# Kernel optimization log

Hardware: AMD Instinct MI355X
Metric: run time of the kernel (lower is better)

The kernel has to match this reference:

```python
import jax, jax.numpy as jnp
import numpy as np

DIM = 768
NUM_HEADS = 12
HEAD_DIM = DIM // NUM_HEADS
SCALE = HEAD_DIM ** -0.5


def setup_inputs() -> dict:
    key = jax.random.key(0)
    k1, k2, k3 = jax.random.split(key, 3)
    B, N = 4, 2048
    x = jax.random.normal(k1, (B, N, DIM), dtype=jnp.float32)
    qkv_w = jax.random.normal(k2, (3 * DIM, DIM), dtype=jnp.float32) * (DIM ** -0.5)
    proj_w = jax.random.normal(k3, (DIM, DIM), dtype=jnp.float32) * (DIM ** -0.5)
    proj_b = jnp.zeros((DIM,), dtype=jnp.float32)
    return {"x": x, "qkv_w": qkv_w, "proj_w": proj_w, "proj_b": proj_b}


def reference(x, qkv_w, proj_w, proj_b):
    B, N, C = x.shape
    # qkv projection (no bias; qkv_bias=False)
    qkv = jnp.einsum('bnc,dc->bnd', x, qkv_w)               # [B,N,3C]
    qkv = qkv.reshape(B, N, 3, NUM_HEADS, HEAD_DIM)
    qkv = jnp.transpose(qkv, (2, 0, 3, 1, 4))               # [3,B,H,N,Dh]
    q, k, v = qkv[0] * SCALE, qkv[1], qkv[2]
    attn = jnp.einsum('bhqd,bhkd->bhqk', q, k)              # [B,H,N,N]
    attn = jax.nn.softmax(attn, axis=-1)
    out = jnp.einsum('bhqk,bhkd->bhqd', attn, v)            # [B,H,N,Dh]
    out = jnp.transpose(out, (0, 2, 1, 3)).reshape(B, N, C)
    out = jnp.einsum('bnc,dc->bnd', out, proj_w) + proj_b
    return out
```

## Files before the change

### kernel.cpp

```cpp
#include <hip/hip_runtime.h>
#include <cstdint>
#include <cstddef>

typedef __attribute__((ext_vector_type(8))) short short8v;
typedef __attribute__((ext_vector_type(4))) float f32x4;
typedef __attribute__((ext_vector_type(16))) float f32x16;
typedef __attribute__((ext_vector_type(4))) unsigned int u32x4;
typedef unsigned short us;

#define GLL16(gsrc, ldst)                                                           \
  __builtin_amdgcn_global_load_lds((__attribute__((address_space(1))) void*)(gsrc), \
                                   (__attribute__((address_space(3))) void*)(ldst), \
                                   16, 0, 0)

#define MFMA32(a, b, c) __builtin_amdgcn_mfma_f32_32x32x16_bf16((a), (b), (c), 0, 0, 0)

static __device__ __forceinline__ us f2bf(float f) {
  unsigned int u = __float_as_uint(f);
  u += 0x7FFFu + ((u >> 16) & 1u);
  return (us)(u >> 16);
}

static __device__ __forceinline__ unsigned int cvtpk_bf16(float lo, float hi) {
  unsigned int r;
  asm("v_cvt_pk_bf16_f32 %0, %1, %2" : "=v"(r) : "v"(lo), "v"(hi));
  return r;
}

template <int B>
static __device__ __forceinline__ short8v pack_swap(const f32x16& p) {
  unsigned int X = cvtpk_bf16(p[B + 0], p[B + 1]);
  unsigned int Y = cvtpk_bf16(p[B + 2], p[B + 3]);
  unsigned int Z = cvtpk_bf16(p[B + 4], p[B + 5]);
  unsigned int W = cvtpk_bf16(p[B + 6], p[B + 7]);
  asm("v_permlane32_swap_b32 %0, %1" : "+v"(X), "+v"(Z));
  asm("v_permlane32_swap_b32 %0, %1" : "+v"(Y), "+v"(W));
  u32x4 f;
  f.x = X; f.y = Y; f.z = Z; f.w = W;
  return __builtin_bit_cast(short8v, f);
}

static __device__ __forceinline__ u32x4 cvt8(const float4 a, const float4 b) {
  u32x4 u;
  u.x = cvtpk_bf16(a.x, a.y);
  u.y = cvtpk_bf16(a.z, a.w);
  u.z = cvtpk_bf16(b.x, b.y);
  u.w = cvtpk_bf16(b.z, b.w);
  return u;
}

__global__ __launch_bounds__(256, 3)
void gemm_qkv(const float* __restrict__ A32, const float* __restrict__ B32,
              int M, int N, int K,
              us* __restrict__ qout, us* __restrict__ kout, us* __restrict__ vtout)
{
  __shared__ us SH[2][2][128 * 32];

  const int tid  = threadIdx.x;
  const int lane = tid & 63;
  const int w    = tid >> 6;
  const int g    = lane >> 4;
  const int c    = lane & 15;
  const int wr   = w >> 1;
  const int wc   = w & 1;
  const int ntn  = N >> 7;

  const int nwg  = (M >> 7) * ntn;
  const int cpx  = nwg >> 3;
  const int bid  = (blockIdx.x & 7) * cpx + (blockIdx.x >> 3);
  const int tm   = bid / ntn;
  const int tn   = bid - tm * ntn;
  const int row_a0 = tm * 128;
  const int col_b0 = tn * 128;

  f32x4 acc[4][4];
#pragma unroll
  for (int i = 0; i < 4; ++i)
#pragma unroll
    for (int j = 0; j < 4; ++j) acc[i][j] = (f32x4){0.f, 0.f, 0.f, 0.f};

  float4 ra[2][2], rb[2][2];

#define STAGE_LOAD(ks)                                                        \
  do {                                                                        \
    _Pragma("unroll")                                                         \
    for (int p = 0; p < 2; ++p) {                                             \
      int G = p * 256 + tid, row = G >> 2, kslot = G & 3;                     \
      const float* s = A32 + (size_t)(row_a0 + row) * K + (ks) * 32 + kslot * 8; \
      ra[p][0] = *(const float4*)s;  ra[p][1] = *(const float4*)(s + 4);      \
    }                                                                         \
    _Pragma("unroll")                                                         \
    for (int p = 0; p < 2; ++p) {                                             \
      int G = p * 256 + tid, row = G >> 2, kslot = G & 3;                     \
      const float* s = B32 + (size_t)(col_b0 + row) * K + (ks) * 32 + kslot * 8; \
      rb[p][0] = *(const float4*)s;  rb[p][1] = *(const float4*)(s + 4);      \
    }                                                                         \
  } while (0)

#define STAGE_WRITE(buf)                                                      \
  do {                                                                        \
    _Pragma("unroll")                                                         \
    for (int p = 0; p < 2; ++p) {                                             \
      int G = p * 256 + tid, row = G >> 2, kslot = G & 3;                     \
      *(u32x4*)&SH[buf][0][(kslot * 128 + row) * 8] = cvt8(ra[p][0], ra[p][1]); \
      *(u32x4*)&SH[buf][1][(kslot * 128 + row) * 8] = cvt8(rb[p][0], rb[p][1]); \
    }                                                                         \
  } while (0)

  const int nt = K >> 5;
  STAGE_LOAD(0);
  STAGE_WRITE(0);
  __syncthreads();

  for (int t = 0; t < nt; ++t) {
    const int cur = t & 1;
    if (t + 1 < nt) STAGE_LOAD(t + 1);

    short8v af[4], bfr[4];
#pragma unroll
    for (int mi = 0; mi < 4; ++mi)
      af[mi] = *(const short8v*)&SH[cur][0][(g * 128 + wr * 64 + mi * 16 + c) * 8];
#pragma unroll
    for (int nj = 0; nj < 4; ++nj)
      bfr[nj] = *(const short8v*)&SH[cur][1][(g * 128 + wc * 64 + nj * 16 + c) * 8];
    __builtin_amdgcn_s_setprio(1);
#pragma unroll
    for (int mi = 0; mi < 4; ++mi)
#pragma unroll
      for (int nj = 0; nj < 4; ++nj)
        acc[mi][nj] = __builtin_amdgcn_mfma_f32_16x16x32_bf16(af[mi], bfr[nj], acc[mi][nj], 0, 0, 0);
    __builtin_amdgcn_s_setprio(0);

    if (t + 1 < nt) STAGE_WRITE(cur ^ 1);
    __syncthreads();
  }
#undef STAGE_LOAD
#undef STAGE_WRITE

  const int rbase = row_a0 + wr * 64;
  const int cbase = col_b0 + wc * 64;
  if (cbase < 1536) {
#pragma unroll
    for (int mi = 0; mi < 4; ++mi)
#pragma unroll
      for (int nj = 0; nj < 4; ++nj)
#pragma unroll
        for (int r = 0; r < 4; ++r) {
          float v   = acc[mi][nj][r];
          int mrow  = rbase + mi * 16 + g * 4 + r;
          int d     = cbase + nj * 16 + c;
          int hh    = d < 768 ? (d >> 6) : ((d - 768) >> 6);
          int dh    = d & 63;
          int b     = mrow >> 11, n = mrow & 2047;
          size_t bh = (size_t)(b * 12 + hh);
          if (d < 768) qout[(bh * 2048 + n) * 64 + dh] = f2bf(v * 0.18033688f);
          else         kout[(bh * 2048 + n) * 64 + dh] = f2bf(v);
        }
  } else {
    us* Lw = &SH[0][0][0] + w * (64 * 40);
    const int b   = rbase >> 11;
    const int nl0 = rbase & 2047;
    const int h2  = (cbase - 1536) >> 6;
    const size_t vrow0 = ((size_t)(b * 12 + h2)) * 64;
#pragma unroll
    for (int pass = 0; pass < 2; ++pass) {
#pragma unroll
      for (int mi2 = 0; mi2 < 2; ++mi2) {
        int mi = pass * 2 + mi2;
#pragma unroll
        for (int nj = 0; nj < 4; ++nj)
#pragma unroll
          for (int r = 0; r < 4; ++r)
            Lw[(nj * 16 + c) * 40 + mi2 * 16 + g * 4 + r] = f2bf(acc[mi][nj][r]);
      }
#pragma unroll
      for (int p = 0; p < 4; ++p) {
        int G   = p * 64 + lane;
        int dl  = G >> 2;
        int seg = G & 3;
        short8v vv = *(const short8v*)&Lw[dl * 40 + seg * 8];
        *(short8v*)(vtout + (vrow0 + dl) * 2048 + nl0 + pass * 32 + seg * 8) = vv;
      }
    }
  }
}

__global__ __launch_bounds__(256, 3)
void gemm_proj(const us* __restrict__ A, const float* __restrict__ B32,
               int M, int N, int K,
               const float* __restrict__ bias, float* __restrict__ fout)
{
  __shared__ us SH[2][2][128 * 32];

  const int tid  = threadIdx.x;
  const int lane = tid & 63;
  const int w    = tid >> 6;
  const int g    = lane >> 4;
  const int c    = lane & 15;
  const int wr   = w >> 1;
  const int wc   = w & 1;
  const int ntn  = N >> 7;

  const int nwg  = (M >> 7) * ntn;
  const int cpx  = nwg >> 3;
  const int bid  = (blockIdx.x & 7) * cpx + (blockIdx.x >> 3);
  const int tm   = bid / ntn;
  const int tn   = bid - tm * ntn;
  const int row_a0 = tm * 128;
  const int col_b0 = tn * 128;

  f32x4 acc[4][4];
#pragma unroll
  for (int i = 0; i < 4; ++i)
#pragma unroll
    for (int j = 0; j < 4; ++j) acc[i][j] = (f32x4){0.f, 0.f, 0.f, 0.f};

  float4 rb[2][2];

#define STAGE_A(buf, ks)                                                      \
  do {                                                                        \
    _Pragma("unroll")                                                         \
    for (int p = 0; p < 2; ++p) {                                             \
      int G = p * 256 + tid;                                                  \
      int kslot = G >> 7, row = G & 127;                                      \
      GLL16(A + (size_t)(row_a0 + row) * K + (ks) * 32 + kslot * 8,           \
            &SH[buf][0][G * 8]);                                              \
    }                                                                         \
  } while (0)

#define STAGE_B_LOAD(ks)                                                      \
  do {                                                                        \
    _Pragma("unroll")                                                         \
    for (int p = 0; p < 2; ++p) {                                             \
      int G = p * 256 + tid, row = G >> 2, kslot = G & 3;                     \
      const float* s = B32 + (size_t)(col_b0 + row) * K + (ks) * 32 + kslot * 8; \
      rb[p][0] = *(const float4*)s;  rb[p][1] = *(const float4*)(s + 4);      \
    }                                                                         \
  } while (0)

#define STAGE_B_WRITE(buf)                                                    \
  do {                                                                        \
    _Pragma("unroll")                                                         \
    for (int p = 0; p < 2; ++p) {                                             \
      int G = p * 256 + tid, row = G >> 2, kslot = G & 3;                     \
      *(u32x4*)&SH[buf][1][(kslot * 128 + row) * 8] = cvt8(rb[p][0], rb[p][1]); \
    }                                                                         \
  } while (0)

  const int nt = K >> 5;
  STAGE_A(0, 0);
  STAGE_B_LOAD(0);
  STAGE_B_WRITE(0);
  __syncthreads();

  for (int t = 0; t < nt; ++t) {
    const int cur = t & 1;
    if (t + 1 < nt) { STAGE_A(cur ^ 1, t + 1); STAGE_B_LOAD(t + 1); }

    short8v af[4], bfr[4];
#pragma unroll
    for (int mi = 0; mi < 4; ++mi)
      af[mi] = *(const short8v*)&SH[cur][0][(g * 128 + wr * 64 + mi * 16 + c) * 8];
#pragma unroll
    for (int nj = 0; nj < 4; ++nj)
      bfr[nj] = *(const short8v*)&SH[cur][1][(g * 128 + wc * 64 + nj * 16 + c) * 8];
    __builtin_amdgcn_s_setprio(1);
#pragma unroll
    for (int mi = 0; mi < 4; ++mi)
#pragma unroll
      for (int nj = 0; nj < 4; ++nj)
        acc[mi][nj] = __builtin_amdgcn_mfma_f32_16x16x32_bf16(af[mi], bfr[nj], acc[mi][nj], 0, 0, 0);
    __builtin_amdgcn_s_setprio(0);

    if (t + 1 < nt) STAGE_B_WRITE(cur ^ 1);
    __syncthreads();
  }
#undef STAGE_A
#undef STAGE_B_LOAD
#undef STAGE_B_WRITE

  const int rbase = row_a0 + wr * 64;
  const int cbase = col_b0 + wc * 64;
#pragma unroll
  for (int mi = 0; mi < 4; ++mi)
#pragma unroll
    for (int nj = 0; nj < 4; ++nj) {
      int d = cbase + nj * 16 + c;
      float bv = bias[d];
#pragma unroll
      for (int r = 0; r < 4; ++r) {
        int mrow = rbase + mi * 16 + g * 4 + r;
        fout[(size_t)mrow * N + d] = acc[mi][nj][r] + bv;
      }
    }
}

__global__ __launch_bounds__(256, 3)
void attn_fwd(const us* __restrict__ Qg, const us* __restrict__ Kg,
              const us* __restrict__ Vg, us* __restrict__ Og)
{
  __shared__ us Ks[2][8 * 64 * 8];
  __shared__ us Vs[2][8 * 64 * 8];

  const int tid  = threadIdx.x;
  const int lane = tid & 63;
  const int w    = tid >> 6;
  const int q31  = lane & 31;
  const int hi   = lane >> 5;

  const int lin = blockIdx.x;
  const int xcd = lin & 7;
  const int idx = lin >> 3;
  const int bh  = xcd * 6 + (idx >> 4);
  const int qt  = idx & 15;
  const int b   = bh / 12;
  const int h   = bh - b * 12;

  const size_t qrow0 = (size_t)bh * 2048 + qt * 128 + w * 32;

  short8v qf[4];
#pragma unroll
  for (int dc = 0; dc < 4; ++dc)
    qf[dc] = *(const short8v*)(Qg + (qrow0 + q31) * 64 + dc * 16 + hi * 8);

  short8v ones;
#pragma unroll
  for (int j = 0; j < 8; ++j) ones[j] = (short)0x3F80;

  f32x16 o0, o1, ls, z16;
#pragma unroll
  for (int r = 0; r < 16; ++r) { o0[r] = 0.f; o1[r] = 0.f; ls[r] = 0.f; z16[r] = 0.f; }

  const size_t kbase = (size_t)bh * 2048 * 64;
  const size_t vbase = (size_t)bh * 64 * 2048;

#define STAGE_KV(buf, kv0)                                             \
  do {                                                                 \
    _Pragma("unroll")                                                  \
    for (int p = 0; p < 2; ++p) {                                      \
      int G = p * 256 + tid;                                           \
      int kslot = G >> 6, row = G & 63;                                \
      GLL16(Kg + kbase + (size_t)((kv0) + row) * 64 + kslot * 8,       \
            &Ks[buf][(p * 256 + w * 64) * 8]);                         \
    }                                                                  \
    _Pragma("unroll")                                                  \
    for (int p = 0; p < 2; ++p) {                                      \
      int G = p * 256 + tid;                                           \
      int kvslot = G >> 6, dh = G & 63;                                \
      GLL16(Vg + vbase + (size_t)dh * 2048 + (kv0) + kvslot * 8,       \
            &Vs[buf][(p * 256 + w * 64) * 8]);                         \
    }                                                                  \
  } while (0)

  STAGE_KV(0, 0);
  __syncthreads();

  for (int t = 0; t < 32; ++t) {
    const int cur = t & 1;
    if (t < 31) STAGE_KV(cur ^ 1, (t + 1) * 64);

    f32x16 s0, s1;
    __builtin_amdgcn_s_setprio(1);
    {
      const us* kb = &Ks[cur][(hi * 64 + q31) * 8];
      short8v kf0 = *(const short8v*)kb;
      short8v kf1 = *(const short8v*)(kb + 32 * 8);
      s0 = MFMA32(kf0, qf[0], z16);
      s1 = MFMA32(kf1, qf[0], z16);
    }
#pragma unroll
    for (int dc = 1; dc < 4; ++dc) {
      const us* kb = &Ks[cur][((dc * 2 + hi) * 64 + q31) * 8];
      short8v kf0 = *(const short8v*)kb;
      short8v kf1 = *(const short8v*)(kb + 32 * 8);
      s0 = MFMA32(kf0, qf[dc], s0);
      s1 = MFMA32(kf1, qf[dc], s1);
    }
    __builtin_amdgcn_s_setprio(0);

#pragma unroll
    for (int r = 0; r < 16; ++r) {
      s0[r] = __builtin_amdgcn_exp2f(s0[r]);
      s1[r] = __builtin_amdgcn_exp2f(s1[r]);
    }

    short8v pa[4];
    pa[0] = pack_swap<0>(s0);
    pa[1] = pack_swap<8>(s0);
    pa[2] = pack_swap<0>(s1);
    pa[3] = pack_swap<8>(s1);

    __builtin_amdgcn_s_setprio(1);
#pragma unroll
    for (int kc = 0; kc < 4; ++kc) {
      const us* vb = &Vs[cur][((kc * 2 + hi) * 64 + q31) * 8];
      short8v vf0 = *(const short8v*)vb;
      short8v vf1 = *(const short8v*)(vb + 32 * 8);
      o0 = MFMA32(pa[kc], vf0, o0);
      o1 = MFMA32(pa[kc], vf1, o1);
      ls = MFMA32(pa[kc], ones, ls);
    }
    __builtin_amdgcn_s_setprio(0);

    __syncthreads();
  }
#undef STAGE_KV

  const int n0w = qt * 128 + w * 32;
#pragma unroll
  for (int r = 0; r < 16; ++r) {
    float iv = 1.0f / ls[r];
    int n = n0w + (r & 3) + 8 * (r >> 2) + 4 * hi;
    size_t rowbase = ((size_t)b * 2048 + n) * 768 + h * 64 + q31;
    Og[rowbase]      = f2bf(o0[r] * iv);
    Og[rowbase + 32] = f2bf(o1[r] * iv);
  }
}

extern "C" void kernel_launch(void* const* d_in, const int* in_sizes, int n_in,
                              void* d_out, int out_size, void* d_ws, size_t ws_size,
                              hipStream_t stream)
{
  const float* x      = (const float*)d_in[0];
  const float* qkv_w  = (const float*)d_in[1];
  const float* proj_w = (const float*)d_in[2];
  const float* proj_b = (const float*)d_in[3];

  char* ws = (char*)d_ws;
  const size_t SZ_AO   = (size_t)8192 * 768 * 2;
  const size_t SZ_HEAD = (size_t)48 * 2048 * 64;

  us* attn_o = (us*)(ws);
  us* q_bf   = (us*)(ws + SZ_AO);
  us* k_bf   = q_bf + SZ_HEAD;
  us* vt_bf  = k_bf + SZ_HEAD;

  gemm_qkv<<<64 * 18, 256, 0, stream>>>(x, qkv_w, 8192, 2304, 768,
                                        q_bf, k_bf, vt_bf);

  attn_fwd<<<768, 256, 0, stream>>>(q_bf, k_bf, vt_bf, attn_o);

  gemm_proj<<<64 * 6, 256, 0, stream>>>(attn_o, proj_w, 8192, 768, 768,
                                        proj_b, (float*)d_out);
}
```

Baseline: 155.5 us.

## Pre-convert weights to bf16 once and stream them into LDS directly

Adds a small kernel that converts the qkv and projection weights from fp32 to bf16 in the workspace at the start of each call. Both GEMMs then load their weight tiles with global_load_lds straight into shared memory, with no register staging or per-tile conversion. This halves weight read traffic in the GEMM loops and removes conversion ALU work and register pressure. The qkv GEMM's launch bounds are also raised to 4 waves per SIMD. The cost is one extra kernel launch plus a full conversion pass over both weight matrices on every call.

```diff
diff --git a/kernel.cpp b/kernel.cpp
--- a/kernel.cpp
+++ b/kernel.cpp
@@ -49,8 +49,21 @@
   return u;
 }
 
-__global__ __launch_bounds__(256, 3)
-void gemm_qkv(const float* __restrict__ A32, const float* __restrict__ B32,
+__global__ void cvt_w(const float4* __restrict__ i0, ushort4* __restrict__ o0, int n0,
+                      const float4* __restrict__ i1, ushort4* __restrict__ o1, int n1)
+{
+  int i = blockIdx.x * 256 + threadIdx.x;
+  const float4* src;
+  ushort4* dst;
+  if (i < n0)           { src = i0;     dst = o0; }
+  else if (i < n0 + n1) { i -= n0;      src = i1; dst = o1; }
+  else return;
+  float4 v = src[i];
+  dst[i] = make_ushort4(f2bf(v.x), f2bf(v.y), f2bf(v.z), f2bf(v.w));
+}
+
+__global__ __launch_bounds__(256, 4)
+void gemm_qkv(const float* __restrict__ A32, const us* __restrict__ Bw,
               int M, int N, int K,
               us* __restrict__ qout, us* __restrict__ kout, us* __restrict__ vtout)
 {
@@ -79,9 +92,9 @@
 #pragma unroll
     for (int j = 0; j < 4; ++j) acc[i][j] = (f32x4){0.f, 0.f, 0.f, 0.f};
 
-  float4 ra[2][2], rb[2][2];
-
-#define STAGE_LOAD(ks)                                                        \
+  float4 ra[2][2];
+
+#define STAGE_A_LOAD(ks)                                                      \
   do {                                                                        \
     _Pragma("unroll")                                                         \
     for (int p = 0; p < 2; ++p) {                                             \
@@ -89,32 +102,37 @@
       const float* s = A32 + (size_t)(row_a0 + row) * K + (ks) * 32 + kslot * 8; \
       ra[p][0] = *(const float4*)s;  ra[p][1] = *(const float4*)(s + 4);      \
     }                                                                         \
-    _Pragma("unroll")                                                         \
-    for (int p = 0; p < 2; ++p) {                                             \
-      int G = p * 256 + tid, row = G >> 2, kslot = G & 3;                     \
-      const float* s = B32 + (size_t)(col_b0 + row) * K + (ks) * 32 + kslot * 8; \
-      rb[p][0] = *(const float4*)s;  rb[p][1] = *(const float4*)(s + 4);      \
-    }                                                                         \
   } while (0)
 
-#define STAGE_WRITE(buf)                                                      \
+#define STAGE_A_WRITE(buf)                                                    \
   do {                                                                        \
     _Pragma("unroll")                                                         \
     for (int p = 0; p < 2; ++p) {                                             \
       int G = p * 256 + tid, row = G >> 2, kslot = G & 3;                     \
       *(u32x4*)&SH[buf][0][(kslot * 128 + row) * 8] = cvt8(ra[p][0], ra[p][1]); \
-      *(u32x4*)&SH[buf][1][(kslot * 128 + row) * 8] = cvt8(rb[p][0], rb[p][1]); \
     }                                                                         \
   } while (0)
 
+#define STAGE_B(buf, ks)                                                      \
+  do {                                                                        \
+    _Pragma("unroll")                                                         \
+    for (int p = 0; p < 2; ++p) {                                             \
+      int G = p * 256 + tid;                                                  \
+      int kslot = G >> 7, row = G & 127;                                      \
+      GLL16(Bw + (size_t)(col_b0 + row) * K + (ks) * 32 + kslot * 8,          \
+            &SH[buf][1][G * 8]);                                              \
+    }                                                                         \
+  } while (0)
+
   const int nt = K >> 5;
-  STAGE_LOAD(0);
-  STAGE_WRITE(0);
+  STAGE_A_LOAD(0);
+  STAGE_B(0, 0);
+  STAGE_A_WRITE(0);
   __syncthreads();
 
   for (int t = 0; t < nt; ++t) {
     const int cur = t & 1;
-    if (t + 1 < nt) STAGE_LOAD(t + 1);
+    if (t + 1 < nt) { STAGE_B(cur ^ 1, t + 1); STAGE_A_LOAD(t + 1); }
 
     short8v af[4], bfr[4];
 #pragma unroll
@@ -131,11 +149,12 @@
         acc[mi][nj] = __builtin_amdgcn_mfma_f32_16x16x32_bf16(af[mi], bfr[nj], acc[mi][nj], 0, 0, 0);
     __builtin_amdgcn_s_setprio(0);
 
-    if (t + 1 < nt) STAGE_WRITE(cur ^ 1);
+    if (t + 1 < nt) STAGE_A_WRITE(cur ^ 1);
     __syncthreads();
   }
-#undef STAGE_LOAD
-#undef STAGE_WRITE
+#undef STAGE_A_LOAD
+#undef STAGE_A_WRITE
+#undef STAGE_B
 
   const int rbase = row_a0 + wr * 64;
   const int cbase = col_b0 + wc * 64;
@@ -186,7 +205,7 @@
 }
 
 __global__ __launch_bounds__(256, 3)
-void gemm_proj(const us* __restrict__ A, const float* __restrict__ B32,
+void gemm_proj(const us* __restrict__ A, const us* __restrict__ Bw,
                int M, int N, int K,
                const float* __restrict__ bias, float* __restrict__ fout)
 {
@@ -215,9 +234,7 @@
 #pragma unroll
     for (int j = 0; j < 4; ++j) acc[i][j] = (f32x4){0.f, 0.f, 0.f, 0.f};
 
-  float4 rb[2][2];
-
-#define STAGE_A(buf, ks)                                                      \
+#define STAGE_AB(buf, ks)                                                     \
   do {                                                                        \
     _Pragma("unroll")                                                         \
     for (int p = 0; p < 2; ++p) {                                             \
@@ -226,36 +243,22 @@
       GLL16(A + (size_t)(row_a0 + row) * K + (ks) * 32 + kslot * 8,           \
             &SH[buf][0][G * 8]);                                              \
     }                                                                         \
-  } while (0)
-
-#define STAGE_B_LOAD(ks)                                                      \
-  do {                                                                        \
     _Pragma("unroll")                                                         \
     for (int p = 0; p < 2; ++p) {                                             \
-      int G = p * 256 + tid, row = G >> 2, kslot = G & 3;                     \
-      const float* s = B32 + (size_t)(col_b0 + row) * K + (ks) * 32 + kslot * 8; \
-      rb[p][0] = *(const float4*)s;  rb[p][1] = *(const float4*)(s + 4);      \
+      int G = p * 256 + tid;                                                  \
+      int kslot = G >> 7, row = G & 127;                                      \
+      GLL16(Bw + (size_t)(col_b0 + row) * K + (ks) * 32 + kslot * 8,          \
+            &SH[buf][1][G * 8]);                                              \
     }                                                                         \
   } while (0)
 
-#define STAGE_B_WRITE(buf)                                                    \
-  do {                                                                        \
-    _Pragma("unroll")                                                         \
-    for (int p = 0; p < 2; ++p) {                                             \
-      int G = p * 256 + tid, row = G >> 2, kslot = G & 3;                     \
-      *(u32x4*)&SH[buf][1][(kslot * 128 + row) * 8] = cvt8(rb[p][0], rb[p][1]); \
-    }                                                                         \
-  } while (0)
-
   const int nt = K >> 5;
-  STAGE_A(0, 0);
-  STAGE_B_LOAD(0);
-  STAGE_B_WRITE(0);
+  STAGE_AB(0, 0);
   __syncthreads();
 
   for (int t = 0; t < nt; ++t) {
     const int cur = t & 1;
-    if (t + 1 < nt) { STAGE_A(cur ^ 1, t + 1); STAGE_B_LOAD(t + 1); }
+    if (t + 1 < nt) STAGE_AB(cur ^ 1, t + 1);
 
     short8v af[4], bfr[4];
 #pragma unroll
@@ -272,12 +275,9 @@
         acc[mi][nj] = __builtin_amdgcn_mfma_f32_16x16x32_bf16(af[mi], bfr[nj], acc[mi][nj], 0, 0, 0);
     __builtin_amdgcn_s_setprio(0);
 
-    if (t + 1 < nt) STAGE_B_WRITE(cur ^ 1);
     __syncthreads();
   }
-#undef STAGE_A
-#undef STAGE_B_LOAD
-#undef STAGE_B_WRITE
+#undef STAGE_AB
 
   const int rbase = row_a0 + wr * 64;
   const int cbase = col_b0 + wc * 64;
@@ -428,18 +428,27 @@
 
   char* ws = (char*)d_ws;
   const size_t SZ_AO   = (size_t)8192 * 768 * 2;
+  const size_t SZ_WQKV = (size_t)2304 * 768 * 2;
+  const size_t SZ_WP   = (size_t)768 * 768 * 2;
   const size_t SZ_HEAD = (size_t)48 * 2048 * 64;
 
   us* attn_o = (us*)(ws);
-  us* q_bf   = (us*)(ws + SZ_AO);
+  us* wqkv   = (us*)(ws + SZ_AO);
+  us* wproj  = (us*)(ws + SZ_AO + SZ_WQKV);
+  us* q_bf   = (us*)(ws + SZ_AO + SZ_WQKV + SZ_WP);
   us* k_bf   = q_bf + SZ_HEAD;
   us* vt_bf  = k_bf + SZ_HEAD;
 
-  gemm_qkv<<<64 * 18, 256, 0, stream>>>(x, qkv_w, 8192, 2304, 768,
+  const int n0 = 2304 * 768 / 4, n1 = 768 * 768 / 4;
+  cvt_w<<<(n0 + n1 + 255) / 256, 256, 0, stream>>>(
+      (const float4*)qkv_w, (ushort4*)wqkv, n0,
+      (const float4*)proj_w, (ushort4*)wproj, n1);
+
+  gemm_qkv<<<64 * 18, 256, 0, stream>>>(x, wqkv, 8192, 2304, 768,
                                         q_bf, k_bf, vt_bf);
 
   attn_fwd<<<768, 256, 0, stream>>>(q_bf, k_bf, vt_bf, attn_o);
 
-  gemm_proj<<<64 * 6, 256, 0, stream>>>(attn_o, proj_w, 8192, 768, 768,
+  gemm_proj<<<64 * 6, 256, 0, stream>>>(attn_o, wproj, 8192, 768, 768,
                                         proj_b, (float*)d_out);
 }
```

After: 172.6 us. 11.0% more time.
